# Performance work log

Hardware: AMD Instinct MI355X
Metric: run time of the kernel (lower is better)

Reference implementation:

```python
import jax, jax.numpy as jnp
import numpy as np


def setup_inputs() -> dict:
    key = jax.random.key(0)
    B, S, N, D = 4, 512, 8, 256
    ks = jax.random.split(key, 5)
    s = 0.02
    inp = {"x": jax.random.normal(ks[0], (B, S, N, D), jnp.float32)}
    for k, name in zip(ks[1:], ["Wq", "Wk", "Wv", "Wo"]):
        inp[name] = jax.random.normal(k, (D, D), jnp.float32) * s
    for name in ["bq", "bk", "bv", "bo"]:
        inp[name] = jnp.zeros((D,), jnp.float32)
    inp["gamma"] = jnp.ones((D,), jnp.float32)
    inp["beta"] = jnp.zeros((D,), jnp.float32)
    inp["num_heads"] = 8
    return inp


def reference(x, Wq, bq, Wk, bk, Wv, bv, Wo, bo, gamma, beta, num_heads):
    B, S, N, D = x.shape
    H = num_heads
    hd = D // H
    # sinusoidal positional encoding: even dims sin, odd dims cos
    pos = jnp.arange(S, dtype=jnp.float32)[:, None]                      # (S,1)
    div = jnp.exp(jnp.arange(0, D, 2, dtype=jnp.float32) * (-np.log(10000.0) / D))
    ang = pos * div                                                       # (S, D/2)
    pe = jnp.stack([jnp.sin(ang), jnp.cos(ang)], axis=-1).reshape(S, D)   # (S, D)
    x_pos = x + pe[None, :, None, :]                                      # (B,S,N,D)
    # fold sensors into batch: (B*N, S, D)
    xr = x_pos.transpose(0, 2, 1, 3).reshape(B * N, S, D)

    def proj(W, b):
        y = xr @ W.T + b                                                  # torch Linear
        return y.reshape(B * N, S, H, hd).transpose(0, 2, 1, 3)          # (BN,H,S,hd)

    Q, K, V = proj(Wq, bq), proj(Wk, bk), proj(Wv, bv)
    scores = jnp.einsum('bhqd,bhkd->bhqk', Q, K) / np.sqrt(hd)            # (BN,H,S,S)
    causal = jnp.tril(jnp.ones((S, S), dtype=bool))
    scores = jnp.where(causal[None, None], scores, jnp.float32(-1e9))
    attn = jax.nn.softmax(scores, axis=-1)                                # dropout = eval mode
    out = jnp.einsum('bhqk,bhkd->bhqd', attn, V)                          # (BN,H,S,hd)
    out = out.transpose(0, 2, 1, 3).reshape(B * N, S, D)
    out = out @ Wo.T + bo
    out = out.reshape(B, N, S, D).transpose(0, 2, 1, 3)                   # (B,S,N,D)
    y = out + x
    mu = jnp.mean(y, axis=-1, keepdims=True)
    var = jnp.var(y, axis=-1, keepdims=True)
    return (y - mu) / jnp.sqrt(var + 1e-5) * gamma + beta
```

## Files before the change

### kernel.cpp

```cpp
#include <hip/hip_runtime.h>
#include <hip/hip_bf16.h>
#include <math.h>

#define B_   4
#define S_   512
#define N_   8
#define D_   256
#define H_   8
#define HD_  32
#define BN_  32
#define MTOT (BN_ * S_)

typedef __attribute__((ext_vector_type(8))) short short8;
typedef __attribute__((ext_vector_type(4))) short short4v;
typedef __attribute__((ext_vector_type(4))) float floatx4;

#define QSCALE 0.25503468f

__device__ __forceinline__ unsigned short f2bf(float f) {
    union { float f; unsigned u; } c; c.f = f;
    unsigned lsb = (c.u >> 16) & 1u;
    c.u += 0x7fffu + lsb;
    return (unsigned short)(c.u >> 16);
}
__device__ __forceinline__ unsigned short f2bf_ru(float f) {
    union { float f; unsigned u; } c; c.f = f;
    return (unsigned short)((c.u + 0x8000u) >> 16);
}
__device__ __forceinline__ float fexp2(float x) {
    float r; asm("v_exp_f32 %0, %1" : "=v"(r) : "v"(x)); return r;
}

__global__ __launch_bounds__(256) void prep_kernel(const float* __restrict__ x,
                                                   const float* __restrict__ Wq,
                                                   const float* __restrict__ Wk,
                                                   const float* __restrict__ Wv,
                                                   const float* __restrict__ Wo,
                                                   unsigned short* __restrict__ xpos,
                                                   unsigned short* __restrict__ wdst) {
    int bid = blockIdx.x;
    if (bid < 4096) {
        int idx4 = bid * 256 + threadIdx.x;
        int d0 = (idx4 << 2) & (D_ - 1);
        int s  = (idx4 >> 6) & (S_ - 1);
        int bn = idx4 >> 15;
        int b = bn >> 3, n = bn & 7;
        floatx4 xv = *(const floatx4*)(x + ((((size_t)b * S_ + s) * N_ + n) << 8) + d0);
        const float cfreq = -9.210340371976184f / 256.0f;
        float f0 = __expf((float)d0 * cfreq);
        float f1 = __expf((float)(d0 + 2) * cfreq);
        float a0 = (float)s * f0, a1 = (float)s * f1;
        short4v o;
        o[0] = (short)f2bf(xv[0] + __sinf(a0));
        o[1] = (short)f2bf(xv[1] + __cosf(a0));
        o[2] = (short)f2bf(xv[2] + __sinf(a1));
        o[3] = (short)f2bf(xv[3] + __cosf(a1));
        *(short4v*)(xpos + ((size_t)idx4 << 2)) = o;
    } else {
        int idx = (bid - 4096) * 256 + threadIdx.x;
        int which = idx >> 16, off = idx & 65535;
        const float* W = (which == 0) ? Wq : (which == 1) ? Wk : (which == 2) ? Wv : Wo;
        wdst[idx] = f2bf(W[off]);
    }
}

__global__ __launch_bounds__(256) void gemm_qkv_kernel(const unsigned short* __restrict__ A,
                                                       const unsigned short* __restrict__ W,
                                                       const float* __restrict__ bq,
                                                       const float* __restrict__ bk,
                                                       const float* __restrict__ bv,
                                                       unsigned short* __restrict__ Qh,
                                                       unsigned short* __restrict__ Kh,
                                                       unsigned short* __restrict__ Vt) {
    int wv = threadIdx.x >> 6, lane = threadIdx.x & 63;
    int col = lane & 15, quad = lane >> 4;
    int m_w = blockIdx.x * 128 + (wv >> 1) * 64;
    int n_w = blockIdx.y * 128 + (wv & 1) * 64;

    const short8* Ap = (const short8*)(A + (size_t)(m_w + col) * 256 + quad * 8);
    const short8* Bp = (const short8*)(W + (size_t)(n_w + col) * 256 + quad * 8);

    floatx4 acc[4][4] = {};
#pragma unroll
    for (int kk = 0; kk < 8; ++kk) {
        short8 a[4], b[4];
#pragma unroll
        for (int t = 0; t < 4; ++t) {
            a[t] = Ap[t * 512 + kk * 4];
            b[t] = Bp[t * 512 + kk * 4];
        }
#pragma unroll
        for (int mt = 0; mt < 4; ++mt)
#pragma unroll
            for (int nt = 0; nt < 4; ++nt)
                acc[mt][nt] = __builtin_amdgcn_mfma_f32_16x16x32_bf16(a[mt], b[nt], acc[mt][nt], 0, 0, 0);
    }

    int sel = blockIdx.y >> 1;
    const float* bias = (sel == 0) ? bq : (sel == 1) ? bk : bv;
#pragma unroll
    for (int nt = 0; nt < 4; ++nt) {
        int c = n_w + nt * 16 + col - sel * 256;
        float bv_ = bias[c];
#pragma unroll
        for (int mt = 0; mt < 4; ++mt) {
            int m0 = m_w + mt * 16 + quad * 4;
            int bn = m0 >> 9, s0 = m0 & (S_ - 1);
            if (sel == 2) {
                short4v pack;
#pragma unroll
                for (int r = 0; r < 4; ++r) pack[r] = (short)f2bf(acc[mt][nt][r] + bv_);
                *(short4v*)(Vt + (((size_t)((bn << 8) + c)) << 9) + s0) = pack;
            } else {
                int h2 = c >> 5, dl = c & 31;
                unsigned short* dst = ((sel == 0) ? Qh : Kh)
                    + ((((size_t)(bn * 8 + h2)) * 512 + s0) << 5) + dl;
                if (sel == 0) {
#pragma unroll
                    for (int r = 0; r < 4; ++r)
                        dst[r << 5] = f2bf((acc[mt][nt][r] + bv_) * QSCALE);
                } else {
#pragma unroll
                    for (int r = 0; r < 4; ++r)
                        dst[r << 5] = f2bf(acc[mt][nt][r] + bv_);
                }
            }
        }
    }
}

__global__ __launch_bounds__(1024) void fattn_kernel(const unsigned short* __restrict__ Qh,
                                                     const unsigned short* __restrict__ Kh,
                                                     const unsigned short* __restrict__ Vt,
                                                     unsigned short* __restrict__ O) {
    __shared__ unsigned short Klds[16384];
    __shared__ unsigned short Vlds[16384];
    __shared__ unsigned short Plds[16][512];

    int t = threadIdx.x;
    int bnh = blockIdx.x;
    int bn = bnh >> 3, h = bnh & 7;
    int wv = t >> 6, lane = t & 63;
    int col = lane & 15, quad = lane >> 4;
    unsigned short* P = &Plds[wv][0];
    int qts[2] = { wv, 31 - wv };

    short8 qf[2];
#pragma unroll
    for (int ui = 0; ui < 2; ++ui)
        qf[ui] = *(const short8*)(Qh + (((size_t)(bnh * S_ + qts[ui] * 16 + col)) << 5) + quad * 8);

    const unsigned short* Ksrc = Kh + ((size_t)bnh << 14);
    const unsigned short* Vsrc = Vt + ((size_t)bnh << 14);
#pragma unroll
    for (int i = 0; i < 2; ++i) {
        int g = t + i * 1024;
        int kt = g >> 7, r = g & 127;
        int half = r >> 6, lin = r & 63;
        int c = lin & 15, q = lin >> 4;
        *(short8*)&Klds[(kt << 10) + (half << 9) + (lin << 3)] =
            *(const short8*)(Ksrc + ((kt * 32 + half * 16 + c) << 5) + (q << 3));
        *(short8*)&Vlds[(kt << 10) + (half << 9) + (lin << 3)] =
            *(const short8*)(Vsrc + (((half << 4) + c) << 9) + (kt << 5) + (q << 3));
    }
    __syncthreads();

#pragma unroll
    for (int ui = 0; ui < 2; ++ui) {
        int q0 = qts[ui] * 16;
        short8 qfrag = qf[ui];
        float l = 0.f;
        floatx4 o0 = {0.f, 0.f, 0.f, 0.f};
        floatx4 o1 = {0.f, 0.f, 0.f, 0.f};
        int lastk = q0 >> 5;

        for (int kt = 0; kt <= lastk; ++kt) {
            int k0 = kt * 32;
            int tb = kt << 10;
            short8 kf0 = *(const short8*)&Klds[tb + (lane << 3)];
            short8 kf1 = *(const short8*)&Klds[tb + 512 + (lane << 3)];
            floatx4 z = {0.f, 0.f, 0.f, 0.f};
            floatx4 st0 = __builtin_amdgcn_mfma_f32_16x16x32_bf16(kf0, qfrag, z, 0, 0, 0);
            floatx4 st1 = __builtin_amdgcn_mfma_f32_16x16x32_bf16(kf1, qfrag, z, 0, 0, 0);

            if (kt == lastk) {
                int qg = q0 + col;
#pragma unroll
                for (int r = 0; r < 4; ++r) {
                    if (k0 + quad * 4 + r > qg)      st0[r] = -1e30f;
                    if (k0 + 16 + quad * 4 + r > qg) st1[r] = -1e30f;
                }
            }

            float p[8]; float ts = 0.f;
#pragma unroll
            for (int r = 0; r < 4; ++r) {
                p[r]     = fexp2(st0[r]);
                p[4 + r] = fexp2(st1[r]);
                ts += p[r] + p[4 + r];
            }
            ts += __shfl_xor(ts, 16);
            ts += __shfl_xor(ts, 32);
            l += ts;

            short4v pk0, pk1;
#pragma unroll
            for (int r = 0; r < 4; ++r) {
                pk0[r] = (short)f2bf_ru(p[r]);
                pk1[r] = (short)f2bf_ru(p[4 + r]);
            }
            int qh_ = quad >> 1, ql_ = (quad & 1) << 2;
            *(short4v*)&P[(((qh_) * 16 + col) << 3) + ql_]     = pk0;
            *(short4v*)&P[(((2 + qh_) * 16 + col) << 3) + ql_] = pk1;
            short8 pfrag = *(const short8*)&P[lane << 3];

            short8 vf0 = *(const short8*)&Vlds[tb + (lane << 3)];
            short8 vf1 = *(const short8*)&Vlds[tb + 512 + (lane << 3)];
            o0 = __builtin_amdgcn_mfma_f32_16x16x32_bf16(vf0, pfrag, o0, 0, 0, 0);
            o1 = __builtin_amdgcn_mfma_f32_16x16x32_bf16(vf1, pfrag, o1, 0, 0, 0);
        }

        float inv = 1.0f / l;
        unsigned short* Op = O + (((size_t)(bn * S_ + q0 + col)) << 8) + h * HD_;
        short4v s0v, s1v;
#pragma unroll
        for (int r = 0; r < 4; ++r) {
            s0v[r] = (short)f2bf(o0[r] * inv);
            s1v[r] = (short)f2bf(o1[r] * inv);
        }
        *(short4v*)(Op + quad * 4)      = s0v;
        *(short4v*)(Op + 16 + quad * 4) = s1v;
    }
}

__global__ __launch_bounds__(256) void gemm_o_ln_kernel(const unsigned short* __restrict__ A,
                                                        const unsigned short* __restrict__ W,
                                                        const float* __restrict__ bo,
                                                        const float* __restrict__ x,
                                                        const float* __restrict__ gamma,
                                                        const float* __restrict__ beta,
                                                        float* __restrict__ out) {
    __shared__ float lsum[4][64];
    __shared__ float lss[4][64];
    __shared__ float lmu[64];
    __shared__ float lrs[64];

    int wv = threadIdx.x >> 6, lane = threadIdx.x & 63;
    int col = lane & 15, quad = lane >> 4;
    int m_b = blockIdx.x * 64;
    int n_w = wv * 64;

    const short8* Ap = (const short8*)(A + (size_t)(m_b + col) * 256 + quad * 8);
    const short8* Bp = (const short8*)(W + (size_t)(n_w + col) * 256 + quad * 8);

    floatx4 acc[4][4] = {};
#pragma unroll
    for (int kk = 0; kk < 8; ++kk) {
        short8 a[4], b[4];
#pragma unroll
        for (int t = 0; t < 4; ++t) {
            a[t] = Ap[t * 512 + kk * 4];
            b[t] = Bp[t * 512 + kk * 4];
        }
#pragma unroll
        for (int mt = 0; mt < 4; ++mt)
#pragma unroll
            for (int nt = 0; nt < 4; ++nt)
                acc[mt][nt] = __builtin_amdgcn_mfma_f32_16x16x32_bf16(a[mt], b[nt], acc[mt][nt], 0, 0, 0);
    }

    int bn = m_b >> 9, s0 = m_b & (S_ - 1);
    int b_ = bn >> 3, n_ = bn & 7;
    const float* xrow = x + ((((size_t)b_ * S_ + s0) * N_ + n_) << 8);
    float* orow = out + ((((size_t)b_ * S_ + s0) * N_ + n_) << 8);

    float psum[4][4] = {};
    float pss[4][4]  = {};
#pragma unroll
    for (int nt = 0; nt < 4; ++nt) {
        int c = n_w + nt * 16 + col;
        float bv_ = bo[c];
#pragma unroll
        for (int mt = 0; mt < 4; ++mt) {
            int sl = mt * 16 + quad * 4;
#pragma unroll
            for (int r = 0; r < 4; ++r) {
                float y = acc[mt][nt][r] + bv_ + xrow[(size_t)(sl + r) * 2048 + c];
                acc[mt][nt][r] = y;
                psum[mt][r] += y;
                pss[mt][r]  += y * y;
            }
        }
    }
#pragma unroll
    for (int off = 8; off >= 1; off >>= 1) {
#pragma unroll
        for (int mt = 0; mt < 4; ++mt)
#pragma unroll
            for (int r = 0; r < 4; ++r) {
                psum[mt][r] += __shfl_xor(psum[mt][r], off);
                pss[mt][r]  += __shfl_xor(pss[mt][r], off);
            }
    }
    if (col == 0) {
#pragma unroll
        for (int mt = 0; mt < 4; ++mt)
#pragma unroll
            for (int r = 0; r < 4; ++r) {
                lsum[wv][mt * 16 + quad * 4 + r] = psum[mt][r];
                lss[wv][mt * 16 + quad * 4 + r]  = pss[mt][r];
            }
    }
    __syncthreads();
    if (threadIdx.x < 64) {
        int row = threadIdx.x;
        float s  = lsum[0][row] + lsum[1][row] + lsum[2][row] + lsum[3][row];
        float ss = lss[0][row] + lss[1][row] + lss[2][row] + lss[3][row];
        float mu = s * (1.0f / 256.0f);
        float var = ss * (1.0f / 256.0f) - mu * mu;
        lmu[row] = mu;
        lrs[row] = rsqrtf(var + 1e-5f);
    }
    __syncthreads();

#pragma unroll
    for (int nt = 0; nt < 4; ++nt) {
        int c = n_w + nt * 16 + col;
        float g  = gamma[c];
        float be = beta[c];
#pragma unroll
        for (int mt = 0; mt < 4; ++mt) {
            int sl = mt * 16 + quad * 4;
#pragma unroll
            for (int r = 0; r < 4; ++r)
                orow[(size_t)(sl + r) * 2048 + c] =
                    (acc[mt][nt][r] - lmu[sl + r]) * lrs[sl + r] * g + be;
        }
    }
}

extern "C" void kernel_launch(void* const* d_in, const int* in_sizes, int n_in,
                              void* d_out, int out_size, void* d_ws, size_t ws_size,
                              hipStream_t stream) {
    const float* x     = (const float*)d_in[0];
    const float* Wq    = (const float*)d_in[1];
    const float* Wk    = (const float*)d_in[2];
    const float* Wv    = (const float*)d_in[3];
    const float* Wo    = (const float*)d_in[4];
    const float* bq    = (const float*)d_in[5];
    const float* bk    = (const float*)d_in[6];
    const float* bv    = (const float*)d_in[7];
    const float* bo    = (const float*)d_in[8];
    const float* gamma = (const float*)d_in[9];
    const float* beta  = (const float*)d_in[10];

    char* w = (char*)d_ws;
    const size_t SZ = (size_t)MTOT * D_ * 2;
    unsigned short* xpos = (unsigned short*)(w);
    unsigned short* Qh   = (unsigned short*)(w + SZ);
    unsigned short* Kh   = (unsigned short*)(w + 2 * SZ);
    unsigned short* Vt   = (unsigned short*)(w + 3 * SZ);
    unsigned short* Ab   = (unsigned short*)(w + 4 * SZ);
    unsigned short* Wbf  = (unsigned short*)(w + 5 * SZ);

    prep_kernel<<<5120, 256, 0, stream>>>(x, Wq, Wk, Wv, Wo, xpos, Wbf);
    gemm_qkv_kernel<<<dim3(128, 6), 256, 0, stream>>>(xpos, Wbf, bq, bk, bv, Qh, Kh, Vt);
    fattn_kernel<<<256, 1024, 0, stream>>>(Qh, Kh, Vt, Ab);
    gemm_o_ln_kernel<<<256, 256, 0, stream>>>(Ab, Wbf + 3 * 65536, bo, x, gamma, beta, (float*)d_out);
}
```

Before: 148.4 us.

## Stage QKV A tile in LDS via direct loads and coalesce LN output stores

The QKV GEMM now gives each block a full 256-column tile, so the grid has half as many blocks. The A tile (128x256 bf16, 64KB) is loaded once into LDS with global_load_lds and shared by all waves, and each wave computes 64x128 with a doubled accumulator. The output/LayerNorm kernel stages normalized rows in padded LDS and then writes them as coalesced float4 stores instead of scattered scalar stores. The cost is higher LDS use and register pressure, which limits occupancy, plus fewer blocks to spread across the CUs.

Result: no change. 150.8 us (+1.6%).

```diff
diff --git a/kernel.cpp b/kernel.cpp
--- a/kernel.cpp
+++ b/kernel.cpp
@@ -29,6 +29,11 @@
 }
 __device__ __forceinline__ float fexp2(float x) {
     float r; asm("v_exp_f32 %0, %1" : "=v"(r) : "v"(x)); return r;
+}
+__device__ __forceinline__ void gload_lds16(const void* g, void* l) {
+    __builtin_amdgcn_global_load_lds(
+        (const __attribute__((address_space(1))) unsigned int*)g,
+        (__attribute__((address_space(3))) unsigned int*)l, 16, 0, 0);
 }
 
 __global__ __launch_bounds__(256) void prep_kernel(const float* __restrict__ x,
@@ -64,47 +69,56 @@
     }
 }
 
-__global__ __launch_bounds__(256) void gemm_qkv_kernel(const unsigned short* __restrict__ A,
-                                                       const unsigned short* __restrict__ W,
-                                                       const float* __restrict__ bq,
-                                                       const float* __restrict__ bk,
-                                                       const float* __restrict__ bv,
-                                                       unsigned short* __restrict__ Qh,
-                                                       unsigned short* __restrict__ Kh,
-                                                       unsigned short* __restrict__ Vt) {
+__global__ __launch_bounds__(256, 2) void gemm_qkv_kernel(const unsigned short* __restrict__ A,
+                                                          const unsigned short* __restrict__ W,
+                                                          const float* __restrict__ bq,
+                                                          const float* __restrict__ bk,
+                                                          const float* __restrict__ bv,
+                                                          unsigned short* __restrict__ Qh,
+                                                          unsigned short* __restrict__ Kh,
+                                                          unsigned short* __restrict__ Vt) {
+    __shared__ __align__(16) unsigned short Alds[32768];
     int wv = threadIdx.x >> 6, lane = threadIdx.x & 63;
     int col = lane & 15, quad = lane >> 4;
-    int m_w = blockIdx.x * 128 + (wv >> 1) * 64;
-    int n_w = blockIdx.y * 128 + (wv & 1) * 64;
-
-    const short8* Ap = (const short8*)(A + (size_t)(m_w + col) * 256 + quad * 8);
-    const short8* Bp = (const short8*)(W + (size_t)(n_w + col) * 256 + quad * 8);
-
-    floatx4 acc[4][4] = {};
+    int m_b = blockIdx.x * 128;
+    int sel = blockIdx.y;
+    int m_w = (wv >> 1) * 64;
+    int n_l = (wv & 1) * 128;
+
+    for (int c = wv * 16; c < wv * 16 + 16; ++c) {
+        int mt = c >> 3, kk = c & 7;
+        const unsigned short* gp = A + (size_t)(m_b + mt * 16 + col) * 256 + kk * 32 + quad * 8;
+        gload_lds16(gp, &Alds[c << 9]);
+    }
+    __syncthreads();
+
+    const short8* Bp = (const short8*)(W + ((size_t)(sel * 256 + n_l + col)) * 256 + quad * 8);
+
+    floatx4 acc[4][8] = {};
 #pragma unroll
     for (int kk = 0; kk < 8; ++kk) {
-        short8 a[4], b[4];
-#pragma unroll
-        for (int t = 0; t < 4; ++t) {
-            a[t] = Ap[t * 512 + kk * 4];
+        short8 a[4], b[8];
+#pragma unroll
+        for (int t = 0; t < 4; ++t)
+            a[t] = *(const short8*)&Alds[((((m_w >> 4) + t) << 3) + kk) << 9 | (lane << 3)];
+#pragma unroll
+        for (int t = 0; t < 8; ++t)
             b[t] = Bp[t * 512 + kk * 4];
-        }
 #pragma unroll
         for (int mt = 0; mt < 4; ++mt)
 #pragma unroll
-            for (int nt = 0; nt < 4; ++nt)
+            for (int nt = 0; nt < 8; ++nt)
                 acc[mt][nt] = __builtin_amdgcn_mfma_f32_16x16x32_bf16(a[mt], b[nt], acc[mt][nt], 0, 0, 0);
     }
 
-    int sel = blockIdx.y >> 1;
     const float* bias = (sel == 0) ? bq : (sel == 1) ? bk : bv;
 #pragma unroll
-    for (int nt = 0; nt < 4; ++nt) {
-        int c = n_w + nt * 16 + col - sel * 256;
+    for (int nt = 0; nt < 8; ++nt) {
+        int c = n_l + nt * 16 + col;
         float bv_ = bias[c];
 #pragma unroll
         for (int mt = 0; mt < 4; ++mt) {
-            int m0 = m_w + mt * 16 + quad * 4;
+            int m0 = m_b + m_w + mt * 16 + quad * 4;
             int bn = m0 >> 9, s0 = m0 & (S_ - 1);
             if (sel == 2) {
                 short4v pack;
@@ -233,6 +247,7 @@
     }
 }
 
+#define YSTR 260
 __global__ __launch_bounds__(256) void gemm_o_ln_kernel(const unsigned short* __restrict__ A,
                                                         const unsigned short* __restrict__ W,
                                                         const float* __restrict__ bo,
@@ -240,6 +255,7 @@
                                                         const float* __restrict__ gamma,
                                                         const float* __restrict__ beta,
                                                         float* __restrict__ out) {
+    __shared__ __align__(16) float Yl[64 * YSTR];
     __shared__ float lsum[4][64];
     __shared__ float lss[4][64];
     __shared__ float lmu[64];
@@ -333,9 +349,17 @@
             int sl = mt * 16 + quad * 4;
 #pragma unroll
             for (int r = 0; r < 4; ++r)
-                orow[(size_t)(sl + r) * 2048 + c] =
-                    (acc[mt][nt][r] - lmu[sl + r]) * lrs[sl + r] * g + be;
-        }
+                Yl[(sl + r) * YSTR + c] = (acc[mt][nt][r] - lmu[sl + r]) * lrs[sl + r] * g + be;
+        }
+    }
+    __syncthreads();
+
+#pragma unroll
+    for (int i = 0; i < 16; ++i) {
+        int linear = i * 1024 + threadIdx.x * 4;
+        int row = linear >> 8, c4 = linear & 255;
+        floatx4 v = *(const floatx4*)&Yl[row * YSTR + c4];
+        *(floatx4*)&orow[(size_t)row * 2048 + c4] = v;
     }
 }
 
@@ -364,7 +388,7 @@
     unsigned short* Wbf  = (unsigned short*)(w + 5 * SZ);
 
     prep_kernel<<<5120, 256, 0, stream>>>(x, Wq, Wk, Wv, Wo, xpos, Wbf);
-    gemm_qkv_kernel<<<dim3(128, 6), 256, 0, stream>>>(xpos, Wbf, bq, bk, bv, Qh, Kh, Vt);
+    gemm_qkv_kernel<<<dim3(128, 3), 256, 0, stream>>>(xpos, Wbf, bq, bk, bv, Qh, Kh, Vt);
     fattn_kernel<<<256, 1024, 0, stream>>>(Qh, Kh, Vt, Ab);
     gemm_o_ln_kernel<<<256, 256, 0, stream>>>(Ab, Wbf + 3 * 65536, bo, x, gamma, beta, (float*)d_out);
 }
```

## Stage output-projection tile in LDS for row-wise vectorized LayerNorm epilogue

Applied to the files above, without the earlier changes.

The GEMM accumulators are written to a padded shared-memory tile, and each wave then processes full 256-wide rows. The residual add, bias, LayerNorm statistics and output happen with float4 loads and stores, plus one wavefront shuffle reduction per row. This replaces the scattered scalar strided global reads and writes of x and out, and the two-stage cross-wave reduction. In exchange the kernel needs about 66KB of LDS per block, which may lower occupancy, and an extra LDS round trip.

Result: no change. 147.8 us (-0.4%).

```diff
diff --git a/kernel.cpp b/kernel.cpp
--- a/kernel.cpp
+++ b/kernel.cpp
@@ -233,6 +233,7 @@
     }
 }
 
+#define YSTR 260
 __global__ __launch_bounds__(256) void gemm_o_ln_kernel(const unsigned short* __restrict__ A,
                                                         const unsigned short* __restrict__ W,
                                                         const float* __restrict__ bo,
@@ -240,10 +241,7 @@
                                                         const float* __restrict__ gamma,
                                                         const float* __restrict__ beta,
                                                         float* __restrict__ out) {
-    __shared__ float lsum[4][64];
-    __shared__ float lss[4][64];
-    __shared__ float lmu[64];
-    __shared__ float lrs[64];
+    __shared__ __align__(16) float Yl[64 * YSTR];
 
     int wv = threadIdx.x >> 6, lane = threadIdx.x & 63;
     int col = lane & 15, quad = lane >> 4;
@@ -269,73 +267,53 @@
                 acc[mt][nt] = __builtin_amdgcn_mfma_f32_16x16x32_bf16(a[mt], b[nt], acc[mt][nt], 0, 0, 0);
     }
 
+#pragma unroll
+    for (int nt = 0; nt < 4; ++nt) {
+        int c = n_w + nt * 16 + col;
+#pragma unroll
+        for (int mt = 0; mt < 4; ++mt) {
+            int sl = mt * 16 + quad * 4;
+#pragma unroll
+            for (int r = 0; r < 4; ++r)
+                Yl[(sl + r) * YSTR + c] = acc[mt][nt][r];
+        }
+    }
+    __syncthreads();
+
     int bn = m_b >> 9, s0 = m_b & (S_ - 1);
     int b_ = bn >> 3, n_ = bn & 7;
     const float* xrow = x + ((((size_t)b_ * S_ + s0) * N_ + n_) << 8);
     float* orow = out + ((((size_t)b_ * S_ + s0) * N_ + n_) << 8);
 
-    float psum[4][4] = {};
-    float pss[4][4]  = {};
-#pragma unroll
-    for (int nt = 0; nt < 4; ++nt) {
-        int c = n_w + nt * 16 + col;
-        float bv_ = bo[c];
-#pragma unroll
-        for (int mt = 0; mt < 4; ++mt) {
-            int sl = mt * 16 + quad * 4;
-#pragma unroll
-            for (int r = 0; r < 4; ++r) {
-                float y = acc[mt][nt][r] + bv_ + xrow[(size_t)(sl + r) * 2048 + c];
-                acc[mt][nt][r] = y;
-                psum[mt][r] += y;
-                pss[mt][r]  += y * y;
-            }
-        }
-    }
-#pragma unroll
-    for (int off = 8; off >= 1; off >>= 1) {
-#pragma unroll
-        for (int mt = 0; mt < 4; ++mt)
-#pragma unroll
-            for (int r = 0; r < 4; ++r) {
-                psum[mt][r] += __shfl_xor(psum[mt][r], off);
-                pss[mt][r]  += __shfl_xor(pss[mt][r], off);
-            }
-    }
-    if (col == 0) {
-#pragma unroll
-        for (int mt = 0; mt < 4; ++mt)
-#pragma unroll
-            for (int r = 0; r < 4; ++r) {
-                lsum[wv][mt * 16 + quad * 4 + r] = psum[mt][r];
-                lss[wv][mt * 16 + quad * 4 + r]  = pss[mt][r];
-            }
-    }
-    __syncthreads();
-    if (threadIdx.x < 64) {
-        int row = threadIdx.x;
-        float s  = lsum[0][row] + lsum[1][row] + lsum[2][row] + lsum[3][row];
-        float ss = lss[0][row] + lss[1][row] + lss[2][row] + lss[3][row];
-        float mu = s * (1.0f / 256.0f);
-        float var = ss * (1.0f / 256.0f) - mu * mu;
-        lmu[row] = mu;
-        lrs[row] = rsqrtf(var + 1e-5f);
-    }
-    __syncthreads();
-
-#pragma unroll
-    for (int nt = 0; nt < 4; ++nt) {
-        int c = n_w + nt * 16 + col;
-        float g  = gamma[c];
-        float be = beta[c];
-#pragma unroll
-        for (int mt = 0; mt < 4; ++mt) {
-            int sl = mt * 16 + quad * 4;
-#pragma unroll
-            for (int r = 0; r < 4; ++r)
-                orow[(size_t)(sl + r) * 2048 + c] =
-                    (acc[mt][nt][r] - lmu[sl + r]) * lrs[sl + r] * g + be;
-        }
+    floatx4 g4  = *(const floatx4*)(gamma + (lane << 2));
+    floatx4 be4 = *(const floatx4*)(beta  + (lane << 2));
+    floatx4 bo4 = *(const floatx4*)(bo    + (lane << 2));
+
+#pragma unroll
+    for (int i = 0; i < 16; ++i) {
+        int row = i * 4 + wv;
+        floatx4 yv = *(const floatx4*)&Yl[row * YSTR + (lane << 2)];
+        floatx4 xv = *(const floatx4*)&xrow[(size_t)row * 2048 + (lane << 2)];
+        float s = 0.f, ss = 0.f;
+#pragma unroll
+        for (int j = 0; j < 4; ++j) {
+            yv[j] += xv[j] + bo4[j];
+            s  += yv[j];
+            ss += yv[j] * yv[j];
+        }
+#pragma unroll
+        for (int off = 1; off <= 32; off <<= 1) {
+            s  += __shfl_xor(s, off);
+            ss += __shfl_xor(ss, off);
+        }
+        float mu   = s * (1.0f / 256.0f);
+        float var  = ss * (1.0f / 256.0f) - mu * mu;
+        float rstd = rsqrtf(var + 1e-5f);
+        floatx4 o;
+#pragma unroll
+        for (int j = 0; j < 4; ++j)
+            o[j] = (yv[j] - mu) * rstd * g4[j] + be4[j];
+        *(floatx4*)&orow[(size_t)row * 2048 + (lane << 2)] = o;
     }
 }
 
```
